# Performance work log

Measured on AMD Instinct MI355X. Metric: run time of the kernel, lower is better.

## Reference

```python
import jax, jax.numpy as jnp
import numpy as np

N = 10000        # nodes
E = 160000       # edges
IN = 1024        # in_channels
OUT = 512        # out_channels
H = 2 * OUT      # hidden width of conv1
EPS = 1e-5
NEG_SLOPE = 0.1


def setup_inputs() -> dict:
    key = jax.random.key(0)
    ks = jax.random.split(key, 8)
    s_in = 1.0 / np.sqrt(IN)
    s_h = 1.0 / np.sqrt(H)
    return {
        "x": jax.random.normal(ks[0], (N, IN), jnp.float32),
        "edge_index": jax.random.randint(ks[1], (2, E), 0, N, dtype=jnp.int64),
        "W1": jax.random.normal(ks[2], (IN, H), jnp.float32) * s_in,
        "b1": jnp.zeros((H,), jnp.float32),
        "Wm": jax.random.normal(ks[3], (H, OUT), jnp.float32) * s_h,
        "bm": jnp.zeros((OUT,), jnp.float32),
        "Ws": jax.random.normal(ks[4], (H, OUT), jnp.float32) * s_h,
        "bs": jnp.zeros((OUT,), jnp.float32),
        "gn_weight": jnp.ones((IN,), jnp.float32),
        "gn_bias": jnp.zeros((IN,), jnp.float32),
        "gn_mean_scale": jnp.ones((IN,), jnp.float32),
    }


def reference(x, edge_index, W1, b1, Wm, bm, Ws, bs, gn_weight, gn_bias, gn_mean_scale):
    # --- GraphNorm (eval, single graph: stats over all nodes) ---
    mean = jnp.mean(x, axis=0)                       # [IN]
    xc = x - gn_mean_scale * mean                    # [N, IN]
    var = jnp.mean(xc * xc, axis=0)                  # [IN]
    x = xc * jax.lax.rsqrt(var + EPS) * gn_weight + gn_bias

    # --- GCN normalization: add self loops, symmetric degree norm ---
    loop = jnp.arange(N, dtype=edge_index.dtype)
    src = jnp.concatenate([edge_index[0], loop])     # [E+N]
    dst = jnp.concatenate([edge_index[1], loop])     # [E+N]
    deg = jax.ops.segment_sum(jnp.ones_like(dst, dtype=x.dtype), dst, num_segments=N)
    deg_inv_sqrt = jax.lax.rsqrt(deg)                # deg >= 1 due to self loops
    enorm = deg_inv_sqrt[src] * deg_inv_sqrt[dst]    # [E+N]

    def gcn_conv(h, W, b):
        h = h @ W                                                        # dense GEMM
        agg = jax.ops.segment_sum(h[src] * enorm[:, None], dst, num_segments=N)
        return agg + b

    h = jax.nn.leaky_relu(gcn_conv(x, W1, b1), NEG_SLOPE)                # [N, H]
    mu = gcn_conv(h, Wm, bm)                                             # [N, OUT]
    logstd = gcn_conv(h, Ws, bs)                                         # [N, OUT]
    z = mu  # eval-mode reparametrize returns mu
    return (z, mu, logstd)
```

## Files before the change

### kernel.cpp

```cpp
#include <hip/hip_runtime.h>
#include <hip/hip_bf16.h>
#include <stdint.h>

#define NNODES 10000
#define NEDGES 160000
#define INCH 1024
#define HCH 1024
#define OUTCH 512
#define MPAD 10112
#define EPSV 1e-5f
#define NEG 0.1f
#define NSB 625
#define NSB2 32

typedef unsigned short u16;
typedef __bf16 bf16x8 __attribute__((ext_vector_type(8)));
typedef float f32x4 __attribute__((ext_vector_type(4)));
typedef __attribute__((address_space(1))) unsigned int gu32;
typedef __attribute__((address_space(3))) unsigned int lu32;

#define GL16(g, l) __builtin_amdgcn_global_load_lds((const gu32*)(g), (lu32*)(l), 16, 0, 0)

__device__ __forceinline__ float bf2f(u16 u) {
    union { unsigned int i; float f; } v; v.i = ((unsigned int)u) << 16; return v.f;
}
__device__ __forceinline__ u16 f2bf(float f) {
    union { float f; unsigned int i; } v; v.f = f;
    unsigned int r = v.i + 0x7fffu + ((v.i >> 16) & 1u);
    return (u16)(r >> 16);
}

__global__ __launch_bounds__(256) void cast_stats_k(const float* __restrict__ x,
                                                    u16* __restrict__ xn,
                                                    float* __restrict__ psum,
                                                    float* __restrict__ psq) {
    int c = threadIdx.x * 4;
    int r0 = blockIdx.x * 16;
    float s0 = 0.f, s1 = 0.f, s2 = 0.f, s3 = 0.f;
    float q0 = 0.f, q1 = 0.f, q2 = 0.f, q3 = 0.f;
#pragma unroll
    for (int r = 0; r < 16; ++r) {
        size_t off = (size_t)(r0 + r) * INCH + c;
        float4 v = *(const float4*)(x + off);
        ushort4 o;
        o.x = f2bf(v.x); o.y = f2bf(v.y); o.z = f2bf(v.z); o.w = f2bf(v.w);
        *(ushort4*)(xn + off) = o;
        float f0 = bf2f(o.x), f1 = bf2f(o.y), f2 = bf2f(o.z), f3 = bf2f(o.w);
        s0 += f0; s1 += f1; s2 += f2; s3 += f3;
        q0 += f0 * f0; q1 += f1 * f1; q2 += f2 * f2; q3 += f3 * f3;
    }
    size_t pb = (size_t)blockIdx.x * 1024 + c;
    *(float4*)(psum + pb) = make_float4(s0, s1, s2, s3);
    *(float4*)(psq + pb)  = make_float4(q0, q1, q2, q3);
}

__global__ __launch_bounds__(256) void reduce1_k(const float* __restrict__ psum,
                                                 const float* __restrict__ psq,
                                                 float* __restrict__ psum2,
                                                 float* __restrict__ psq2) {
    int c = threadIdx.x * 4;
    int b0 = blockIdx.x * 20;
    int b1 = min(b0 + 20, NSB);
    f32x4 s = {0.f, 0.f, 0.f, 0.f}, q = {0.f, 0.f, 0.f, 0.f};
    for (int b = b0; b < b1; ++b) {
        f32x4 vs = *(const f32x4*)(psum + (size_t)b * 1024 + c);
        f32x4 vq = *(const f32x4*)(psq + (size_t)b * 1024 + c);
        s += vs; q += vq;
    }
    *(f32x4*)(psum2 + (size_t)blockIdx.x * 1024 + c) = s;
    *(f32x4*)(psq2 + (size_t)blockIdx.x * 1024 + c) = q;
}

__global__ __launch_bounds__(256) void scale2_k(const float* __restrict__ psum2,
                                                const float* __restrict__ psq2,
                                                const float* __restrict__ gms,
                                                const float* __restrict__ gw,
                                                const float* __restrict__ gb,
                                                float* __restrict__ sc, float* __restrict__ sh) {
    int c = blockIdx.x * 256 + threadIdx.x;
    float s = 0.f, q = 0.f;
#pragma unroll
    for (int b = 0; b < NSB2; ++b) {
        s += psum2[(size_t)b * 1024 + c];
        q += psq2[(size_t)b * 1024 + c];
    }
    const float invn = 1.0f / NNODES;
    float m = s * invn;
    float msq = q * invn;
    float g = gms[c];
    float var = msq - g * (2.0f - g) * m * m;
    float scale = rsqrtf(var + EPSV) * gw[c];
    sc[c] = scale;
    sh[c] = gb[c] - g * m * scale;
}

__global__ void c1_k(const float* __restrict__ W1, const float* __restrict__ sh,
                     float* __restrict__ c1) {
    int j = blockIdx.x * 256 + threadIdx.x;
    int k0 = blockIdx.y * 128;
    float a = 0.f;
#pragma unroll 4
    for (int k = k0; k < k0 + 128; ++k) a += sh[k] * W1[(size_t)k * HCH + j];
    atomicAdd(&c1[j], a);
}

__global__ __launch_bounds__(256) void wt1_k(const float* __restrict__ W,
                                             const float* __restrict__ sc,
                                             u16* __restrict__ Bt) {
    __shared__ u16 t[64][68];
    int k0 = blockIdx.y * 64, c0 = blockIdx.x * 64;
    int tc = (threadIdx.x & 15) * 4;
    int tk = threadIdx.x >> 4;
#pragma unroll
    for (int i = 0; i < 64; i += 16) {
        float scr = sc[k0 + tk + i];
        float4 v = *(const float4*)(W + (size_t)(k0 + tk + i) * HCH + c0 + tc);
        t[tc + 0][tk + i] = f2bf(v.x * scr);
        t[tc + 1][tk + i] = f2bf(v.y * scr);
        t[tc + 2][tk + i] = f2bf(v.z * scr);
        t[tc + 3][tk + i] = f2bf(v.w * scr);
    }
    __syncthreads();
    int wk = (threadIdx.x & 15) * 4;
    int wc = threadIdx.x >> 4;
#pragma unroll
    for (int i = 0; i < 64; i += 16) {
        ushort4 o;
        o.x = t[wc + i][wk + 0]; o.y = t[wc + i][wk + 1];
        o.z = t[wc + i][wk + 2]; o.w = t[wc + i][wk + 3];
        *(ushort4*)(Bt + (size_t)(c0 + wc + i) * 1024 + k0 + wk) = o;
    }
}

__global__ __launch_bounds__(256) void wt2_k(const float* __restrict__ Wm,
                                             const float* __restrict__ Ws,
                                             u16* __restrict__ Bt) {
    __shared__ u16 t[64][68];
    int k0 = blockIdx.y * 64, c0 = blockIdx.x * 64;
    const float* W = (c0 < OUTCH) ? Wm : Ws;
    int cb = (c0 < OUTCH) ? c0 : c0 - OUTCH;
    int tc = (threadIdx.x & 15) * 4;
    int tk = threadIdx.x >> 4;
#pragma unroll
    for (int i = 0; i < 64; i += 16) {
        float4 v = *(const float4*)(W + (size_t)(k0 + tk + i) * OUTCH + cb + tc);
        t[tc + 0][tk + i] = f2bf(v.x);
        t[tc + 1][tk + i] = f2bf(v.y);
        t[tc + 2][tk + i] = f2bf(v.z);
        t[tc + 3][tk + i] = f2bf(v.w);
    }
    __syncthreads();
    int wk = (threadIdx.x & 15) * 4;
    int wc = threadIdx.x >> 4;
#pragma unroll
    for (int i = 0; i < 64; i += 16) {
        ushort4 o;
        o.x = t[wc + i][wk + 0]; o.y = t[wc + i][wk + 1];
        o.z = t[wc + i][wk + 2]; o.w = t[wc + i][wk + 3];
        *(ushort4*)(Bt + (size_t)(c0 + wc + i) * 1024 + k0 + wk) = o;
    }
}

__global__ void deg_k(const int* __restrict__ dst, int* __restrict__ cnt) {
    int e = blockIdx.x * 256 + threadIdx.x;
    if (e < NEDGES) atomicAdd(&cnt[dst[e]], 1);
}
__global__ void dis_k(const int* __restrict__ cnt, float* __restrict__ dis,
                      float* __restrict__ rowsum) {
    int i = blockIdx.x * 256 + threadIdx.x;
    if (i < NNODES) {
        float d = rsqrtf((float)(cnt[i] + 1));
        dis[i] = d;
        rowsum[i] = d * d;
    }
}
__global__ void scan_k(const int* __restrict__ cnt, int* __restrict__ row_ptr,
                       int* __restrict__ cursor) {
    __shared__ int sm[256];
    int tid = threadIdx.x;
    const int per = 40;
    int base = tid * per;
    int s = 0;
    for (int i = 0; i < per; ++i) { int idx = base + i; if (idx < NNODES) s += cnt[idx]; }
    sm[tid] = s; __syncthreads();
    for (int off = 1; off < 256; off <<= 1) {
        int v = (tid >= off) ? sm[tid - off] : 0;
        __syncthreads();
        sm[tid] += v;
        __syncthreads();
    }
    int run = (tid == 0) ? 0 : sm[tid - 1];
    for (int i = 0; i < per; ++i) {
        int idx = base + i;
        if (idx < NNODES) { row_ptr[idx] = run; cursor[idx] = run; run += cnt[idx]; }
    }
    if (tid == 255) row_ptr[NNODES] = sm[255];
}
__global__ void fill_k(const int* __restrict__ src, const int* __restrict__ dst,
                       const float* __restrict__ dis, int* __restrict__ cursor,
                       int2* __restrict__ csr, float* __restrict__ rowsum) {
    int e = blockIdx.x * 256 + threadIdx.x;
    if (e >= NEDGES) return;
    int s = src[e], d = dst[e];
    float w = dis[s] * dis[d];
    int pos = atomicAdd(&cursor[d], 1);
    csr[pos] = make_int2(s, __float_as_int(w));
    atomicAdd(&rowsum[d], w);
}

template<int MODE>
__global__ __launch_bounds__(256) void agg_k(const u16* __restrict__ in, u16* __restrict__ out,
                      const int* __restrict__ row_ptr, const int2* __restrict__ csr,
                      const float* __restrict__ dis,
                      const float* __restrict__ bias, const float* __restrict__ rowsum,
                      const float* __restrict__ c1) {
    int node = blockIdx.x;
    int c = threadIdx.x * 4;
    float dv = dis[node];
    float selfw = dv * dv;
    const size_t base = 0;
    ushort4 sv = *(const ushort4*)(in + (size_t)node * HCH + c);
    f32x4 a0 = {bf2f(sv.x) * selfw, bf2f(sv.y) * selfw, bf2f(sv.z) * selfw, bf2f(sv.w) * selfw};
    f32x4 a1 = {0.f, 0.f, 0.f, 0.f};
    f32x4 a2 = {0.f, 0.f, 0.f, 0.f};
    f32x4 a3 = {0.f, 0.f, 0.f, 0.f};
    int e0 = row_ptr[node], e1 = row_ptr[node + 1];
    int e = e0;
    for (; e + 4 <= e1; e += 4) {
        int2 sw0 = csr[e + 0];
        int2 sw1 = csr[e + 1];
        int2 sw2 = csr[e + 2];
        int2 sw3 = csr[e + 3];
        ushort4 v0 = *(const ushort4*)(in + (size_t)sw0.x * HCH + c);
        ushort4 v1 = *(const ushort4*)(in + (size_t)sw1.x * HCH + c);
        ushort4 v2 = *(const ushort4*)(in + (size_t)sw2.x * HCH + c);
        ushort4 v3 = *(const ushort4*)(in + (size_t)sw3.x * HCH + c);
        float w0 = __int_as_float(sw0.y), w1 = __int_as_float(sw1.y);
        float w2 = __int_as_float(sw2.y), w3 = __int_as_float(sw3.y);
        a0 += (f32x4){bf2f(v0.x), bf2f(v0.y), bf2f(v0.z), bf2f(v0.w)} * w0;
        a1 += (f32x4){bf2f(v1.x), bf2f(v1.y), bf2f(v1.z), bf2f(v1.w)} * w1;
        a2 += (f32x4){bf2f(v2.x), bf2f(v2.y), bf2f(v2.z), bf2f(v2.w)} * w2;
        a3 += (f32x4){bf2f(v3.x), bf2f(v3.y), bf2f(v3.z), bf2f(v3.w)} * w3;
    }
    for (; e < e1; ++e) {
        int2 sw = csr[e];
        float w = __int_as_float(sw.y);
        ushort4 v = *(const ushort4*)(in + (size_t)sw.x * HCH + c);
        a0 += (f32x4){bf2f(v.x), bf2f(v.y), bf2f(v.z), bf2f(v.w)} * w;
    }
    f32x4 a = (a0 + a1) + (a2 + a3);
    if (MODE == 1) {
        float rs = rowsum[node];
        float4 b = *(const float4*)(bias + c);
        float4 cc = *(const float4*)(c1 + c);
        a[0] += rs * cc.x + b.x; a[1] += rs * cc.y + b.y;
        a[2] += rs * cc.z + b.z; a[3] += rs * cc.w + b.w;
        a[0] = a[0] > 0.f ? a[0] : NEG * a[0];
        a[1] = a[1] > 0.f ? a[1] : NEG * a[1];
        a[2] = a[2] > 0.f ? a[2] : NEG * a[2];
        a[3] = a[3] > 0.f ? a[3] : NEG * a[3];
    }
    ushort4 o; o.x = f2bf(a[0]); o.y = f2bf(a[1]); o.z = f2bf(a[2]); o.w = f2bf(a[3]);
    *(ushort4*)(out + (size_t)node * HCH + c) = o;
}

template<int EPI>
__global__ __launch_bounds__(256) void gemm_k(
    const u16* __restrict__ A, const u16* __restrict__ Bt,
    u16* __restrict__ Cbf, float* __restrict__ out,
    const float* __restrict__ bm, const float* __restrict__ bs) {
    __shared__ u16 As[128 * 32];
    __shared__ u16 Bs[128 * 32];
    const int tid = threadIdx.x;
    const int wave = tid >> 6;
    const int lane = tid & 63;
    const int row0 = blockIdx.y * 128;
    const int col0 = blockIdx.x * 128;
    const int wr = wave >> 1, wc = wave & 1;
    const int sr = lane >> 2;
    const int sc = (lane & 3) * 8;
    u16* AsW0 = &As[(wave * 16) * 32];
    u16* AsW1 = &As[(64 + wave * 16) * 32];
    u16* BsW0 = &Bs[(wave * 16) * 32];
    u16* BsW1 = &Bs[(64 + wave * 16) * 32];
    const u16* Ag0 = A + (size_t)(row0 + wave * 16 + sr) * 1024 + sc;
    const u16* Ag1 = A + (size_t)(row0 + 64 + wave * 16 + sr) * 1024 + sc;
    const u16* Bg0 = Bt + (size_t)(col0 + wave * 16 + sr) * 1024 + sc;
    const u16* Bg1 = Bt + (size_t)(col0 + 64 + wave * 16 + sr) * 1024 + sc;

    f32x4 acc[4][4] = {};
    const int arow = lane & 15;
    const int ak = (lane >> 4) * 8;
    for (int kk = 0; kk < 1024; kk += 32) {
        GL16(Ag0 + kk, AsW0);
        GL16(Ag1 + kk, AsW1);
        GL16(Bg0 + kk, BsW0);
        GL16(Bg1 + kk, BsW1);
        __syncthreads();
        bf16x8 af[4], bf[4];
#pragma unroll
        for (int m = 0; m < 4; ++m)
            af[m] = *reinterpret_cast<const bf16x8*>(&As[(wr * 64 + m * 16 + arow) * 32 + ak]);
#pragma unroll
        for (int n = 0; n < 4; ++n)
            bf[n] = *reinterpret_cast<const bf16x8*>(&Bs[(wc * 64 + n * 16 + arow) * 32 + ak]);
#pragma unroll
        for (int m = 0; m < 4; ++m)
#pragma unroll
            for (int n = 0; n < 4; ++n)
                acc[m][n] = __builtin_amdgcn_mfma_f32_16x16x32_bf16(af[m], bf[n], acc[m][n], 0, 0, 0);
        __syncthreads();
    }
    const int crow = (lane >> 4) * 4;
    const int ccol = lane & 15;
    if (EPI == 0) {
#pragma unroll
        for (int m = 0; m < 4; ++m) {
            int rbase = row0 + wr * 64 + m * 16 + crow;
#pragma unroll
            for (int n = 0; n < 4; ++n) {
                int col = col0 + wc * 64 + n * 16 + ccol;
                f32x4 v = acc[m][n];
#pragma unroll
                for (int r = 0; r < 4; ++r)
                    Cbf[(size_t)(rbase + r) * 1024 + col] = f2bf(v[r]);
            }
        }
    } else {
        const size_t NOUT = (size_t)NNODES * OUTCH;
#pragma unroll
        for (int n = 0; n < 4; ++n) {
            int col = col0 + wc * 64 + n * 16 + ccol;
            bool lo = col < OUTCH;
            int colo = lo ? col : col - OUTCH;
            float bias = lo ? bm[colo] : bs[colo];
#pragma unroll
            for (int m = 0; m < 4; ++m) {
                int rbase = row0 + wr * 64 + m * 16 + crow;
                f32x4 v = acc[m][n];
#pragma unroll
                for (int r = 0; r < 4; ++r) {
                    int rr = rbase + r;
                    if (rr < NNODES) {
                        float val = v[r] + bias;
                        if (lo) {
                            out[(size_t)rr * OUTCH + colo] = val;
                            out[NOUT + (size_t)rr * OUTCH + colo] = val;
                        } else {
                            out[2 * NOUT + (size_t)rr * OUTCH + colo] = val;
                        }
                    }
                }
            }
        }
    }
}

extern "C" void kernel_launch(void* const* d_in, const int* in_sizes, int n_in,
                              void* d_out, int out_size, void* d_ws, size_t ws_size,
                              hipStream_t stream) {
    const float* x   = (const float*)d_in[0];
    const int*   ei  = (const int*)d_in[1];
    const float* W1  = (const float*)d_in[2];
    const float* b1  = (const float*)d_in[3];
    const float* Wm  = (const float*)d_in[4];
    const float* bm  = (const float*)d_in[5];
    const float* Ws  = (const float*)d_in[6];
    const float* bs  = (const float*)d_in[7];
    const float* gw  = (const float*)d_in[8];
    const float* gb  = (const float*)d_in[9];
    const float* gms = (const float*)d_in[10];
    const int* srcI = ei;
    const int* dstI = ei + NEDGES;

    char* ws = (char*)d_ws;
    const size_t SBIG = (size_t)MPAD * 1024 * 2;
    u16* xn   = (u16*)(ws);
    u16* h1g  = (u16*)(ws + SBIG);
    u16* h    = (u16*)(ws + 2 * SBIG);
    u16* aggh = xn;
    u16* Bt1  = (u16*)(ws + 3 * SBIG);
    u16* Bt2  = (u16*)(ws + 3 * SBIG + (size_t)2 * 1024 * 1024);
    float* psum  = (float*)(ws + SBIG);
    float* psq   = (float*)(ws + SBIG + (size_t)NSB * 4096);
    float* psum2 = (float*)(ws + SBIG + (size_t)2 * NSB * 4096);
    float* psq2  = (float*)(ws + SBIG + (size_t)2 * NSB * 4096 + (size_t)NSB2 * 4096);
    char* small   = ws + 3 * SBIG + (size_t)4 * 1024 * 1024;
    int*   cnt    = (int*)(small);
    float* rowsum = (float*)(small + 40960);
    float* c1     = (float*)(small + 81920);
    int*   row_ptr= (int*)(small + 86016);
    int*   cursor = (int*)(small + 126976);
    float* dis    = (float*)(small + 167936);
    int2*  csr    = (int2*)(small + 208896);
    float* sc     = (float*)(small + 1488896);
    float* sh     = (float*)(small + 1492992);

    hipMemsetAsync(small, 0, 86016, stream);

    cast_stats_k<<<NSB, 256, 0, stream>>>(x, xn, psum, psq);
    deg_k<<<625, 256, 0, stream>>>(dstI, cnt);
    dis_k<<<40, 256, 0, stream>>>(cnt, dis, rowsum);
    scan_k<<<1, 256, 0, stream>>>(cnt, row_ptr, cursor);
    fill_k<<<625, 256, 0, stream>>>(srcI, dstI, dis, cursor, csr, rowsum);
    reduce1_k<<<NSB2, 256, 0, stream>>>(psum, psq, psum2, psq2);
    scale2_k<<<4, 256, 0, stream>>>(psum2, psq2, gms, gw, gb, sc, sh);
    wt1_k<<<dim3(16, 16), 256, 0, stream>>>(W1, sc, Bt1);
    c1_k<<<dim3(4, 8), 256, 0, stream>>>(W1, sh, c1);
    wt2_k<<<dim3(16, 16), 256, 0, stream>>>(Wm, Ws, Bt2);

    gemm_k<0><<<dim3(8, 79), 256, 0, stream>>>(xn, Bt1, h1g, nullptr, nullptr, nullptr);
    agg_k<1><<<NNODES, 256, 0, stream>>>(h1g, h, row_ptr, csr, dis, b1, rowsum, c1);
    agg_k<0><<<NNODES, 256, 0, stream>>>(h, aggh, row_ptr, csr, dis, nullptr, nullptr, nullptr);
    gemm_k<1><<<dim3(8, 79), 256, 0, stream>>>(aggh, Bt2, nullptr, (float*)d_out, bm, bs);
}
```

Before: 376.1 us.

## Slice aggregation by channel groups and remap GEMM blocks for XCD locality

The aggregation kernel changes from one block per node covering all 1024 channels to a 2D grid: 8 channel slices of 128, with 4 nodes per block and one wave per node. Each slice's working set of gathered rows is smaller, so gathered neighbor data should stay in L2/cache longer. The GEMM launch becomes a 1D grid with a remap that keeps blocks sharing the same row tile together, likely to suit the round-robin distribution of workgroups across XCDs. The trade-off is narrower 4-byte loads per lane and CSR edge lists re-read once per slice.

```diff
diff --git a/kernel.cpp b/kernel.cpp
--- a/kernel.cpp
+++ b/kernel.cpp
@@ -209,21 +209,21 @@
 }
 
 template<int MODE>
-__global__ __launch_bounds__(256) void agg_k(const u16* __restrict__ in, u16* __restrict__ out,
+__global__ __launch_bounds__(256) void aggs_k(const u16* __restrict__ in, u16* __restrict__ out,
                       const int* __restrict__ row_ptr, const int2* __restrict__ csr,
                       const float* __restrict__ dis,
                       const float* __restrict__ bias, const float* __restrict__ rowsum,
                       const float* __restrict__ c1) {
-    int node = blockIdx.x;
-    int c = threadIdx.x * 4;
+    int slice = blockIdx.x;
+    int node = blockIdx.y * 4 + (threadIdx.x >> 6);
+    int lane = threadIdx.x & 63;
+    int ch = slice * 128 + lane * 2;
     float dv = dis[node];
     float selfw = dv * dv;
-    const size_t base = 0;
-    ushort4 sv = *(const ushort4*)(in + (size_t)node * HCH + c);
-    f32x4 a0 = {bf2f(sv.x) * selfw, bf2f(sv.y) * selfw, bf2f(sv.z) * selfw, bf2f(sv.w) * selfw};
-    f32x4 a1 = {0.f, 0.f, 0.f, 0.f};
-    f32x4 a2 = {0.f, 0.f, 0.f, 0.f};
-    f32x4 a3 = {0.f, 0.f, 0.f, 0.f};
+    unsigned int sv = *(const unsigned int*)(in + (size_t)node * HCH + ch);
+    float a0 = bf2f((u16)(sv & 0xffff)) * selfw;
+    float a1 = bf2f((u16)(sv >> 16)) * selfw;
+    float b0 = 0.f, b1v = 0.f, c0 = 0.f, c1v = 0.f, d0 = 0.f, d1 = 0.f, e0a = 0.f, e1a = 0.f;
     int e0 = row_ptr[node], e1 = row_ptr[node + 1];
     int e = e0;
     for (; e + 4 <= e1; e += 4) {
@@ -231,37 +231,36 @@
         int2 sw1 = csr[e + 1];
         int2 sw2 = csr[e + 2];
         int2 sw3 = csr[e + 3];
-        ushort4 v0 = *(const ushort4*)(in + (size_t)sw0.x * HCH + c);
-        ushort4 v1 = *(const ushort4*)(in + (size_t)sw1.x * HCH + c);
-        ushort4 v2 = *(const ushort4*)(in + (size_t)sw2.x * HCH + c);
-        ushort4 v3 = *(const ushort4*)(in + (size_t)sw3.x * HCH + c);
+        unsigned int v0 = *(const unsigned int*)(in + (size_t)sw0.x * HCH + ch);
+        unsigned int v1 = *(const unsigned int*)(in + (size_t)sw1.x * HCH + ch);
+        unsigned int v2 = *(const unsigned int*)(in + (size_t)sw2.x * HCH + ch);
+        unsigned int v3 = *(const unsigned int*)(in + (size_t)sw3.x * HCH + ch);
         float w0 = __int_as_float(sw0.y), w1 = __int_as_float(sw1.y);
         float w2 = __int_as_float(sw2.y), w3 = __int_as_float(sw3.y);
-        a0 += (f32x4){bf2f(v0.x), bf2f(v0.y), bf2f(v0.z), bf2f(v0.w)} * w0;
-        a1 += (f32x4){bf2f(v1.x), bf2f(v1.y), bf2f(v1.z), bf2f(v1.w)} * w1;
-        a2 += (f32x4){bf2f(v2.x), bf2f(v2.y), bf2f(v2.z), bf2f(v2.w)} * w2;
-        a3 += (f32x4){bf2f(v3.x), bf2f(v3.y), bf2f(v3.z), bf2f(v3.w)} * w3;
+        a0 += bf2f((u16)(v0 & 0xffff)) * w0; a1 += bf2f((u16)(v0 >> 16)) * w0;
+        b0 += bf2f((u16)(v1 & 0xffff)) * w1; b1v += bf2f((u16)(v1 >> 16)) * w1;
+        c0 += bf2f((u16)(v2 & 0xffff)) * w2; c1v += bf2f((u16)(v2 >> 16)) * w2;
+        d0 += bf2f((u16)(v3 & 0xffff)) * w3; d1 += bf2f((u16)(v3 >> 16)) * w3;
     }
     for (; e < e1; ++e) {
         int2 sw = csr[e];
         float w = __int_as_float(sw.y);
-        ushort4 v = *(const ushort4*)(in + (size_t)sw.x * HCH + c);
-        a0 += (f32x4){bf2f(v.x), bf2f(v.y), bf2f(v.z), bf2f(v.w)} * w;
-    }
-    f32x4 a = (a0 + a1) + (a2 + a3);
+        unsigned int v = *(const unsigned int*)(in + (size_t)sw.x * HCH + ch);
+        e0a += bf2f((u16)(v & 0xffff)) * w; e1a += bf2f((u16)(v >> 16)) * w;
+    }
+    float r0 = ((a0 + b0) + (c0 + d0)) + e0a;
+    float r1 = ((a1 + b1v) + (c1v + d1)) + e1a;
     if (MODE == 1) {
         float rs = rowsum[node];
-        float4 b = *(const float4*)(bias + c);
-        float4 cc = *(const float4*)(c1 + c);
-        a[0] += rs * cc.x + b.x; a[1] += rs * cc.y + b.y;
-        a[2] += rs * cc.z + b.z; a[3] += rs * cc.w + b.w;
-        a[0] = a[0] > 0.f ? a[0] : NEG * a[0];
-        a[1] = a[1] > 0.f ? a[1] : NEG * a[1];
-        a[2] = a[2] > 0.f ? a[2] : NEG * a[2];
-        a[3] = a[3] > 0.f ? a[3] : NEG * a[3];
-    }
-    ushort4 o; o.x = f2bf(a[0]); o.y = f2bf(a[1]); o.z = f2bf(a[2]); o.w = f2bf(a[3]);
-    *(ushort4*)(out + (size_t)node * HCH + c) = o;
+        float2 bb = *(const float2*)(bias + ch);
+        float2 cc = *(const float2*)(c1 + ch);
+        r0 += rs * cc.x + bb.x;
+        r1 += rs * cc.y + bb.y;
+        r0 = r0 > 0.f ? r0 : NEG * r0;
+        r1 = r1 > 0.f ? r1 : NEG * r1;
+    }
+    unsigned int o = (unsigned int)f2bf(r0) | ((unsigned int)f2bf(r1) << 16);
+    *(unsigned int*)(out + (size_t)node * HCH + ch) = o;
 }
 
 template<int EPI>
@@ -271,11 +270,13 @@
     const float* __restrict__ bm, const float* __restrict__ bs) {
     __shared__ u16 As[128 * 32];
     __shared__ u16 Bs[128 * 32];
+    const int orig = blockIdx.x;
+    const int wg = (orig & 7) * 79 + (orig >> 3);
+    const int row0 = (wg >> 3) * 128;
+    const int col0 = (wg & 7) * 128;
     const int tid = threadIdx.x;
     const int wave = tid >> 6;
     const int lane = tid & 63;
-    const int row0 = blockIdx.y * 128;
-    const int col0 = blockIdx.x * 128;
     const int wr = wave >> 1, wc = wave & 1;
     const int sr = lane >> 2;
     const int sc = (lane & 3) * 8;
@@ -409,8 +410,8 @@
     c1_k<<<dim3(4, 8), 256, 0, stream>>>(W1, sh, c1);
     wt2_k<<<dim3(16, 16), 256, 0, stream>>>(Wm, Ws, Bt2);
 
-    gemm_k<0><<<dim3(8, 79), 256, 0, stream>>>(xn, Bt1, h1g, nullptr, nullptr, nullptr);
-    agg_k<1><<<NNODES, 256, 0, stream>>>(h1g, h, row_ptr, csr, dis, b1, rowsum, c1);
-    agg_k<0><<<NNODES, 256, 0, stream>>>(h, aggh, row_ptr, csr, dis, nullptr, nullptr, nullptr);
-    gemm_k<1><<<dim3(8, 79), 256, 0, stream>>>(aggh, Bt2, nullptr, (float*)d_out, bm, bs);
-}
+    gemm_k<0><<<632, 256, 0, stream>>>(xn, Bt1, h1g, nullptr, nullptr, nullptr);
+    aggs_k<1><<<dim3(8, 2500), 256, 0, stream>>>(h1g, h, row_ptr, csr, dis, b1, rowsum, c1);
+    aggs_k<0><<<dim3(8, 2500), 256, 0, stream>>>(h, aggh, row_ptr, csr, dis, nullptr, nullptr, nullptr);
+    gemm_k<1><<<632, 256, 0, stream>>>(aggh, Bt2, nullptr, (float*)d_out, bm, bs);
+}
```

After: 369.9 us. No clear change (-1.6%).
